# Kernel optimization log

Measured on AMD Instinct MI355X. Metric: run time of the kernel, lower is better.

## Reference

```python
import jax, jax.numpy as jnp
import numpy as np

B, T, W, L, H = 32, 1024, 512, 12, 8
CH = W // H                      # per-head dim = 64
IN_CH = 3 + 6 + T                # x + params + class embedding channels = 1033
DFF = 4 * W
NEG = -100000.0
SCALE = 1.0 / np.sqrt(np.sqrt(CH))


def _layernorm(x, g, b, eps=1e-5):
    m = jnp.mean(x, axis=-1, keepdims=True)
    v = jnp.mean(jnp.square(x - m), axis=-1, keepdims=True)
    return (x - m) * jax.lax.rsqrt(v + eps) * g + b


def setup_inputs() -> dict:
    key = jax.random.key(0)
    ks = jax.random.split(key, 40)
    std = 0.25 * np.sqrt(1.0 / W)  # init_scale used inside Transformer

    def n(k, shape, s=std):
        return (jax.random.normal(k, shape, jnp.float32) * s).astype(jnp.float32)

    inp = {
        'x': jax.random.normal(ks[0], (B, 3, T), jnp.float32),
        'params': jax.random.normal(ks[1], (B, 6, T), jnp.float32),
        'mask': (jax.random.uniform(ks[2], (B, T)) > 0.2).astype(jnp.float32),
        'class_emb': jax.random.normal(ks[3], (T, T), jnp.float32),  # nn.Embedding(n_ctx, n_ctx)
        'w_in': n(ks[4], (IN_CH, W), 0.02), 'b_in': jnp.zeros((W,), jnp.float32),
        'ln_pre_g': jnp.ones((W,), jnp.float32), 'ln_pre_b': jnp.zeros((W,), jnp.float32),
        'qkv_w': n(ks[5], (L, W, 3 * W)), 'qkv_b': jnp.zeros((L, 3 * W), jnp.float32),
        'attn_pw': n(ks[6], (L, W, W)), 'attn_pb': jnp.zeros((L, W), jnp.float32),
        'ln1_g': jnp.ones((L, W), jnp.float32), 'ln1_b': jnp.zeros((L, W), jnp.float32),
        'fc_w': n(ks[7], (L, W, DFF)), 'fc_b': jnp.zeros((L, DFF), jnp.float32),
        'fcp_w': n(ks[8], (L, DFF, W)), 'fcp_b': jnp.zeros((L, W), jnp.float32),
        'ln2_g': jnp.ones((L, W), jnp.float32), 'ln2_b': jnp.zeros((L, W), jnp.float32),
        'ln_post_g': jnp.ones((W,), jnp.float32), 'ln_post_b': jnp.zeros((W,), jnp.float32),
        'w_out': n(ks[9], (W, W), 0.02), 'b_out': jnp.zeros((W,), jnp.float32),
        'agg_fc_w': n(ks[10], (W, DFF)), 'agg_fc_b': jnp.zeros((DFF,), jnp.float32),
        'agg_pw': n(ks[11], (DFF, W)), 'agg_pb': jnp.zeros((W,), jnp.float32),
    }
    return inp


def _block(h, p):
    qw, qb, pw, pb, l1g, l1b, fw, fb, gw, gb, l2g, l2b = p
    hn = _layernorm(h, l1g, l1b)
    qkv = (hn @ qw + qb).reshape(B, T, H, 3 * CH)
    q, k, v = jnp.split(qkv, 3, axis=-1)
    att = jnp.einsum('bthc,bshc->bhts', q * SCALE, k * SCALE)
    att = jax.nn.softmax(att.astype(jnp.float32), axis=-1)  # softmax in fp32
    o = jnp.einsum('bhts,bshc->bthc', att, v).reshape(B, T, W)
    h = h + o @ pw + pb
    hn2 = _layernorm(h, l2g, l2b)
    h = h + jax.nn.gelu(hn2 @ fw + fb, approximate=False) @ gw + gb
    return h, None


def reference(x, params, mask, class_emb, w_in, b_in, ln_pre_g, ln_pre_b,
              qkv_w, qkv_b, attn_pw, attn_pb, ln1_g, ln1_b, fc_w, fc_b,
              fcp_w, fcp_b, ln2_g, ln2_b, ln_post_g, ln_post_b, w_out, b_out,
              agg_fc_w, agg_fc_b, agg_pw, agg_pb):
    # concatenate params and class-embedding channels: [B, 1033, T]
    ce = jnp.broadcast_to(class_emb.T[None], (B, T, T))  # class_embed.transpose(1,2)
    xin = jnp.concatenate([x, params, ce], axis=1)
    h = jnp.einsum('bct,cw->btw', xin, w_in) + b_in      # input_proj on [B,T,1033]
    h = _layernorm(h, ln_pre_g, ln_pre_b)
    h, _ = jax.lax.scan(_block, h,
                        (qkv_w, qkv_b, attn_pw, attn_pb, ln1_g, ln1_b,
                         fc_w, fc_b, fcp_w, fcp_b, ln2_g, ln2_b))
    h = _layernorm(h, ln_post_g, ln_post_b)
    h = (h @ w_out + b_out).transpose(0, 2, 1)           # [B, 512, T]
    h = h * mask[:, None, :]
    pooled = jnp.max(h + (1.0 - mask[:, None, :]) * NEG, axis=2)  # [B, 512]
    z = jax.nn.gelu(pooled @ agg_fc_w + agg_fc_b, approximate=False) @ agg_pw + agg_pb
    return (z, h)
```

## Files before the change

kernel.cpp:

```cpp
#include <hip/hip_runtime.h>
#include <hip/hip_bf16.h>


typedef unsigned short u16;
typedef unsigned int u32;
typedef __attribute__((ext_vector_type(8))) short bf16x8;
typedef __attribute__((ext_vector_type(8))) unsigned short us8;
typedef __attribute__((ext_vector_type(4))) unsigned short us4;
typedef __attribute__((ext_vector_type(4))) float f32x4;

__device__ __forceinline__ float bf2f(u16 s) {
  union { u32 u; float f; } c; c.u = ((u32)s) << 16; return c.f;
}
__device__ __forceinline__ u16 f2bf(float f) {
  __hip_bfloat16 h = __float2bfloat16(f);
  union { __hip_bfloat16 h; u16 u; } c; c.h = h; return c.u;
}
__device__ __forceinline__ float gelu_f(float v) {
  return 0.5f * v * (1.0f + erff(v * 0.7071067811865475f));
}
__device__ __forceinline__ void gl2lds16(const u16* g, u16* l) {
  __builtin_amdgcn_global_load_lds((const __attribute__((address_space(1))) void*)g,
                                   (__attribute__((address_space(3))) void*)l, 16, 0, 0);
}
__device__ __forceinline__ f32x4 mfma16(bf16x8 a, bf16x8 b, f32x4 c) {
  return __builtin_amdgcn_mfma_f32_16x16x32_bf16(a, b, c, 0, 0, 0);
}
__device__ __forceinline__ int swz(int row) { return (row ^ (row >> 3)) & 7; }

template <int EPI>
__global__ __launch_bounds__(512)
void gemm_bt(const u16* __restrict__ A, const u16* __restrict__ Bt,
             const float* __restrict__ bias, float* __restrict__ Cf,
             u16* __restrict__ Cb, u16* __restrict__ Vt, int K, int lda, int ldb, int ldc)
{
  __shared__ __align__(16) u16 As[2][256 * 32];
  __shared__ __align__(16) u16 Bs[2][128 * 32];
  const int tid = threadIdx.x;
  const int lane = tid & 63, wid = tid >> 6;
  const int wm = wid & 3, wn = wid >> 2;
  const int nbx = gridDim.x;
  const int nwg = nbx * gridDim.y;
  int lin = blockIdx.y * nbx + blockIdx.x;
  lin = (lin & 7) * (nwg >> 3) + (lin >> 3);
  const long m0 = (long)(lin / nbx) * 256, n0 = (long)(lin % nbx) * 128;

  const int c0 = tid, c1 = tid + 512;
  const int kc0 = (c0 & 3) ^ (((c0 >> 2) >> 1) & 3);
  const int kc1 = (c1 & 3) ^ (((c1 >> 2) >> 1) & 3);
  const int kcb = (tid & 3) ^ (((tid >> 2) >> 1) & 3);
  const u16* aS0 = A + (m0 + (c0 >> 2)) * (long)lda + kc0 * 8;
  const u16* aS1 = A + (m0 + (c1 >> 2)) * (long)lda + kc1 * 8;
  const u16* bS0 = Bt + (n0 + (tid >> 2)) * (long)ldb + kcb * 8;

  f32x4 acc[4][4] = {};
  const int cl4 = lane & 15;
  const int gph = ((lane >> 4) ^ ((cl4 >> 1) & 3)) * 8;
  const int aro = (wm * 64 + cl4) * 32 + gph;
  const int bro = (wn * 64 + cl4) * 32 + gph;
  const int nt = K >> 5;

#define STAGE_AB(buf, k0_)                          \
  gl2lds16(aS0 + (k0_), As[buf] + c0 * 8);          \
  gl2lds16(aS1 + (k0_), As[buf] + c1 * 8);          \
  gl2lds16(bS0 + (k0_), Bs[buf] + tid * 8);

  STAGE_AB(0, 0);
  for (int t = 0; t < nt; ++t) {
    const int cur = t & 1;
    if (t < nt - 1) {
      STAGE_AB(cur ^ 1, (t + 1) * 32);
      asm volatile("s_waitcnt vmcnt(3)" ::: "memory");
    } else {
      asm volatile("s_waitcnt vmcnt(0)" ::: "memory");
    }
    __builtin_amdgcn_s_barrier();
    bf16x8 af[4], bfr[4];
#pragma unroll
    for (int i = 0; i < 4; ++i) af[i] = *(const bf16x8*)(As[cur] + aro + i * 16 * 32);
#pragma unroll
    for (int j = 0; j < 4; ++j) bfr[j] = *(const bf16x8*)(Bs[cur] + bro + j * 16 * 32);
    __builtin_amdgcn_s_setprio(1);
#pragma unroll
    for (int i = 0; i < 4; ++i)
#pragma unroll
      for (int j = 0; j < 4; ++j)
        acc[i][j] = mfma16(af[i], bfr[j], acc[i][j]);
    __builtin_amdgcn_s_setprio(0);
    __builtin_amdgcn_s_barrier();
  }
#undef STAGE_AB
  const int rg = (lane >> 4) * 4, cl = lane & 15;
#pragma unroll
  for (int i = 0; i < 4; ++i) {
#pragma unroll
    for (int j = 0; j < 4; ++j) {
      const long row = m0 + wm * 64 + i * 16 + rg;
      const long col = n0 + wn * 64 + j * 16 + cl;
      const float bv = bias ? bias[col] : 0.0f;
      if (EPI == 4) {
        const int hh = (int)col / 192, off = (int)col - hh * 192;
        if (off < 64) {
#pragma unroll
          for (int r = 0; r < 4; ++r)
            Cb[(row + r) * ldc + col] = f2bf((acc[i][j][r] + bv) * 0.125f);
        } else if (off < 128) {
#pragma unroll
          for (int r = 0; r < 4; ++r)
            Cb[(row + r) * ldc + col] = f2bf(acc[i][j][r] + bv);
        } else {
          us4 pk;
#pragma unroll
          for (int r = 0; r < 4; ++r) pk[r] = f2bf(acc[i][j][r] + bv);
          const long bl = row >> 10, t0 = row & 1023;
          *(us4*)(Vt + (((bl * 8 + hh) * 64 + (off - 128)) << 10) + t0) = pk;
        }
      } else {
#pragma unroll
        for (int r = 0; r < 4; ++r) {
          float v = acc[i][j][r] + bv;
          long idx = (row + r) * ldc + col;
          if (EPI == 0) Cf[idx] = v;
          else if (EPI == 1) Cb[idx] = f2bf(v);
          else if (EPI == 2) Cf[idx] += v;
          else Cb[idx] = f2bf(gelu_f(v));
        }
      }
    }
  }
}

template <int EPI>
__global__ __launch_bounds__(256)
void gemm_bt1(const u16* __restrict__ A, const u16* __restrict__ Bt,
              const float* __restrict__ bias, float* __restrict__ Cf,
              u16* __restrict__ Cb, int K, int lda, int ldb, int ldc)
{
  __shared__ __align__(16) u16 As[2][128 * 32];
  __shared__ __align__(16) u16 Bs[2][128 * 32];
  const int tid = threadIdx.x;
  const int lane = tid & 63, wid = tid >> 6;
  const int wm = wid >> 1, wn = wid & 1;
  const int nbx = gridDim.x;
  const int nwg = nbx * gridDim.y;
  int lin = blockIdx.y * nbx + blockIdx.x;
  lin = (lin & 7) * (nwg >> 3) + (lin >> 3);
  const long m0 = (long)(lin / nbx) * 128, n0 = (long)(lin % nbx) * 128;

  const int c0 = tid, c1 = tid + 256;
  const int kc0 = (c0 & 3) ^ (((c0 >> 2) >> 1) & 3);
  const int kc1 = (c1 & 3) ^ (((c1 >> 2) >> 1) & 3);
  const u16* aS0 = A + (m0 + (c0 >> 2)) * (long)lda + kc0 * 8;
  const u16* aS1 = A + (m0 + (c1 >> 2)) * (long)lda + kc1 * 8;
  const u16* bS0 = Bt + (n0 + (c0 >> 2)) * (long)ldb + kc0 * 8;
  const u16* bS1 = Bt + (n0 + (c1 >> 2)) * (long)ldb + kc1 * 8;

  f32x4 acc[4][4] = {};
  const int cl4 = lane & 15;
  const int gph = ((lane >> 4) ^ ((cl4 >> 1) & 3)) * 8;
  const int aro = (wm * 64 + cl4) * 32 + gph;
  const int bro = (wn * 64 + cl4) * 32 + gph;
  const int nt = K >> 5;

#define STAGE_AB1(buf, k0_)                         \
  gl2lds16(aS0 + (k0_), As[buf] + c0 * 8);          \
  gl2lds16(aS1 + (k0_), As[buf] + c1 * 8);          \
  gl2lds16(bS0 + (k0_), Bs[buf] + c0 * 8);          \
  gl2lds16(bS1 + (k0_), Bs[buf] + c1 * 8);

  STAGE_AB1(0, 0);
  for (int t = 0; t < nt; ++t) {
    const int cur = t & 1;
    if (t < nt - 1) {
      STAGE_AB1(cur ^ 1, (t + 1) * 32);
      asm volatile("s_waitcnt vmcnt(4)" ::: "memory");
    } else {
      asm volatile("s_waitcnt vmcnt(0)" ::: "memory");
    }
    __builtin_amdgcn_s_barrier();
    bf16x8 af[4], bfr[4];
#pragma unroll
    for (int i = 0; i < 4; ++i) af[i] = *(const bf16x8*)(As[cur] + aro + i * 16 * 32);
#pragma unroll
    for (int j = 0; j < 4; ++j) bfr[j] = *(const bf16x8*)(Bs[cur] + bro + j * 16 * 32);
    __builtin_amdgcn_s_setprio(1);
#pragma unroll
    for (int i = 0; i < 4; ++i)
#pragma unroll
      for (int j = 0; j < 4; ++j)
        acc[i][j] = mfma16(af[i], bfr[j], acc[i][j]);
    __builtin_amdgcn_s_setprio(0);
    __builtin_amdgcn_s_barrier();
  }
#undef STAGE_AB1
  const int rg = (lane >> 4) * 4, cl = lane & 15;
#pragma unroll
  for (int i = 0; i < 4; ++i) {
#pragma unroll
    for (int j = 0; j < 4; ++j) {
      const long row = m0 + wm * 64 + i * 16 + rg;
      const long col = n0 + wn * 64 + j * 16 + cl;
      const float bv = bias ? bias[col] : 0.0f;
#pragma unroll
      for (int r = 0; r < 4; ++r) {
        float v = acc[i][j][r] + bv;
        long idx = (row + r) * ldc + col;
        if (EPI == 0) Cf[idx] = v;
        else if (EPI == 1) Cb[idx] = f2bf(v);
        else if (EPI == 2) Cf[idx] += v;
        else Cb[idx] = f2bf(gelu_f(v));
      }
    }
  }
}

template <int EPI>
__global__ __launch_bounds__(1024)
void gemm_bt2(const u16* __restrict__ A, const u16* __restrict__ Bt,
              const float* __restrict__ bias, float* __restrict__ Cf,
              u16* __restrict__ Cb, int K, int lda, int ldb, int ldc)
{
  __shared__ __align__(16) u16 As[2][256 * 32];
  __shared__ __align__(16) u16 Bs[2][256 * 32];
  const int tid = threadIdx.x;
  const int lane = tid & 63, wid = tid >> 6;
  const int wm = wid & 3, wn = wid >> 2;
  const int nbx = gridDim.x;
  const int nwg = nbx * gridDim.y;
  int lin = blockIdx.y * nbx + blockIdx.x;
  lin = (lin & 7) * (nwg >> 3) + (lin >> 3);
  const long m0 = (long)(lin / nbx) * 256, n0 = (long)(lin % nbx) * 256;

  const int kcA = (tid & 3) ^ (((tid >> 2) >> 1) & 3);
  const u16* aS0 = A + (m0 + (tid >> 2)) * (long)lda + kcA * 8;
  const u16* bS0 = Bt + (n0 + (tid >> 2)) * (long)ldb + kcA * 8;

  f32x4 acc[4][4] = {};
  const int cl4 = lane & 15;
  const int gph = ((lane >> 4) ^ ((cl4 >> 1) & 3)) * 8;
  const int aro = (wm * 64 + cl4) * 32 + gph;
  const int bro = (wn * 64 + cl4) * 32 + gph;
  const int nt = K >> 5;

#define STAGE_AB2(buf, k0_)                         \
  gl2lds16(aS0 + (k0_), As[buf] + tid * 8);         \
  gl2lds16(bS0 + (k0_), Bs[buf] + tid * 8);

  STAGE_AB2(0, 0);
  for (int t = 0; t < nt; ++t) {
    const int cur = t & 1;
    if (t < nt - 1) {
      STAGE_AB2(cur ^ 1, (t + 1) * 32);
      asm volatile("s_waitcnt vmcnt(2)" ::: "memory");
    } else {
      asm volatile("s_waitcnt vmcnt(0)" ::: "memory");
    }
    __builtin_amdgcn_s_barrier();
    bf16x8 af[4], bfr[4];
#pragma unroll
    for (int i = 0; i < 4; ++i) af[i] = *(const bf16x8*)(As[cur] + aro + i * 16 * 32);
#pragma unroll
    for (int j = 0; j < 4; ++j) bfr[j] = *(const bf16x8*)(Bs[cur] + bro + j * 16 * 32);
    __builtin_amdgcn_s_setprio(1);
#pragma unroll
    for (int i = 0; i < 4; ++i)
#pragma unroll
      for (int j = 0; j < 4; ++j)
        acc[i][j] = mfma16(af[i], bfr[j], acc[i][j]);
    __builtin_amdgcn_s_setprio(0);
    __builtin_amdgcn_s_barrier();
  }
#undef STAGE_AB2
  const int rg = (lane >> 4) * 4, cl = lane & 15;
#pragma unroll
  for (int i = 0; i < 4; ++i) {
#pragma unroll
    for (int j = 0; j < 4; ++j) {
      const long row = m0 + wm * 64 + i * 16 + rg;
      const long col = n0 + wn * 64 + j * 16 + cl;
      const float bv = bias ? bias[col] : 0.0f;
#pragma unroll
      for (int r = 0; r < 4; ++r) {
        float v = acc[i][j][r] + bv;
        long idx = (row + r) * ldc + col;
        if (EPI == 0) Cf[idx] = v;
        else if (EPI == 1) Cb[idx] = f2bf(v);
        else if (EPI == 2) Cf[idx] += v;
        else Cb[idx] = f2bf(gelu_f(v));
      }
    }
  }
}

__global__ __launch_bounds__(512)
void attn_k(const u16* __restrict__ qkv, const u16* __restrict__ vt, u16* __restrict__ o)
{
  __shared__ __align__(16) u16 Ks[2][64 * 64];
  __shared__ __align__(16) u16 Vts[2][64 * 64];
  __shared__ __align__(16) u16 Ps[8][512];
  const int tid = threadIdx.x, lane = tid & 63, wid = tid >> 6;
  int lin = blockIdx.x;
  lin = (lin & 7) * 128 + (lin >> 3);
  const int qt = lin & 7, hh = (lin >> 3) & 7, b = lin >> 6;
  const long rowbase = (long)b * 1024;
  const long vbase = (((long)b * 8 + hh) * 64) * 1024;
  const int g = lane >> 4, cl = lane & 15;
  u16* Psw = Ps[wid];
  const int Rq = wid * 16 + cl;
  const int sw2 = ((cl >> 1) & 3) << 3;

  bf16x8 aq[2];
  {
    const u16* qp = qkv + (rowbase + qt * 128 + Rq) * 1536 + hh * 192 + g * 8;
    aq[0] = *(const bf16x8*)(qp);
    aq[1] = *(const bf16x8*)(qp + 32);
  }
#define STAGE_KV(buf, kt_)                                                            \
  {                                                                                   \
    int row = tid >> 3, c8s = (tid & 7) ^ swz(row);                                   \
    gl2lds16(qkv + (rowbase + (kt_) * 64 + row) * 1536 + hh * 192 + 64 + c8s * 8,     \
             Ks[buf] + tid * 8);                                                      \
    gl2lds16(vt + vbase + (long)row * 1024 + (kt_) * 64 + c8s * 8, Vts[buf] + tid * 8); \
  }
  STAGE_KV(0, 0);

  float m = -3.0e38f, l = 0.f;
  f32x4 oacc[4] = {};

  for (int kt = 0; kt < 16; ++kt) {
    const int cur = kt & 1;
    if (kt < 15) {
      STAGE_KV(cur ^ 1, kt + 1);
      asm volatile("s_waitcnt vmcnt(2)" ::: "memory");
    } else {
      asm volatile("s_waitcnt vmcnt(0)" ::: "memory");
    }
    __builtin_amdgcn_s_barrier();
    f32x4 s[4] = {};
    __builtin_amdgcn_s_setprio(1);
#pragma unroll
    for (int j = 0; j < 4; ++j) {
      const int Rk = j * 16 + cl, sk = swz(Rk) << 3;
#pragma unroll
      for (int kb = 0; kb < 2; ++kb) {
        bf16x8 bk = *(const bf16x8*)(Ks[cur] + Rk * 64 + ((kb * 32 + g * 8) ^ sk));
        s[j] = mfma16(bk, aq[kb], s[j]);
      }
    }
    __builtin_amdgcn_s_setprio(0);
    float mx = s[0][0];
#pragma unroll
    for (int j = 0; j < 4; ++j)
#pragma unroll
      for (int r = 0; r < 4; ++r) mx = fmaxf(mx, s[j][r]);
    mx = fmaxf(mx, __shfl_xor(mx, 16, 64));
    mx = fmaxf(mx, __shfl_xor(mx, 32, 64));
    if (!__all(mx <= m + 8.f)) {
      const float mnew = fmaxf(m, mx);
      const float al = __expf(m - mnew);
      m = mnew;
      l *= al;
      float alr[4];
#pragma unroll
      for (int r = 0; r < 4; ++r) alr[r] = __shfl(al, (lane & 48) | (g * 4 + r), 64);
#pragma unroll
      for (int cb = 0; cb < 4; ++cb) {
        f32x4 t = oacc[cb];
        t[0] *= alr[0]; t[1] *= alr[1]; t[2] *= alr[2]; t[3] *= alr[3];
        oacc[cb] = t;
      }
    }
    float p[4][4], ts = 0.f;
#pragma unroll
    for (int j = 0; j < 4; ++j)
#pragma unroll
      for (int r = 0; r < 4; ++r) {
        p[j][r] = __expf(s[j][r] - m);
        ts += p[j][r];
      }
    ts += __shfl_xor(ts, 16, 64);
    ts += __shfl_xor(ts, 32, 64);
    l += ts;
#pragma unroll
    for (int kb = 0; kb < 2; ++kb) {
#pragma unroll
      for (int jj = 0; jj < 2; ++jj) {
        us4 pk;
        pk[0] = f2bf(p[2 * kb + jj][0]); pk[1] = f2bf(p[2 * kb + jj][1]);
        pk[2] = f2bf(p[2 * kb + jj][2]); pk[3] = f2bf(p[2 * kb + jj][3]);
        *(us4*)(&Psw[cl * 32 + ((jj * 16 + g * 4) ^ sw2)]) = pk;
      }
      asm volatile("s_waitcnt lgkmcnt(0)" ::: "memory");
      bf16x8 pa = *(const bf16x8*)(&Psw[cl * 32 + ((g * 8) ^ sw2)]);
      __builtin_amdgcn_s_setprio(1);
#pragma unroll
      for (int cb = 0; cb < 4; ++cb) {
        const int ch = cb * 16 + cl;
        bf16x8 vb = *(const bf16x8*)(Vts[cur] + ch * 64 + ((kb * 32 + g * 8) ^ (swz(ch) << 3)));
        oacc[cb] = mfma16(pa, vb, oacc[cb]);
      }
      __builtin_amdgcn_s_setprio(0);
    }
    __builtin_amdgcn_s_barrier();
  }
#undef STAGE_KV
  float lr[4];
#pragma unroll
  for (int r = 0; r < 4; ++r) lr[r] = __shfl(l, (lane & 48) | (g * 4 + r), 64);
#pragma unroll
  for (int cb = 0; cb < 4; ++cb)
#pragma unroll
    for (int r = 0; r < 4; ++r) {
      long row = rowbase + qt * 128 + wid * 16 + g * 4 + r;
      o[row * 512 + hh * 64 + cb * 16 + cl] = f2bf(oacc[cb][r] / lr[r]);
    }
}

template <int MODE>
__global__ __launch_bounds__(256)
void ln_k(const float* __restrict__ in_, const float* __restrict__ gg,
          const float* __restrict__ bb, void* __restrict__ out_)
{
  const long row = (long)blockIdx.x * 4 + (threadIdx.x >> 6);
  const int lane = threadIdx.x & 63;
  float x[8];
  const float* p = in_ + row * 512 + lane * 8;
  *(float4*)(x) = *(const float4*)(p);
  *(float4*)(x + 4) = *(const float4*)(p + 4);
  float s = 0.f;
#pragma unroll
  for (int j = 0; j < 8; ++j) s += x[j];
#pragma unroll
  for (int off = 1; off < 64; off <<= 1) s += __shfl_xor(s, off, 64);
  const float mean = s * (1.0f / 512.0f);
  float vs = 0.f;
#pragma unroll
  for (int j = 0; j < 8; ++j) { float d = x[j] - mean; vs += d * d; }
#pragma unroll
  for (int off = 1; off < 64; off <<= 1) vs += __shfl_xor(vs, off, 64);
  const float rstd = rsqrtf(vs * (1.0f / 512.0f) + 1e-5f);
  if (MODE == 0) {
    float y[8];
#pragma unroll
    for (int j = 0; j < 8; ++j)
      y[j] = (x[j] - mean) * rstd * gg[lane * 8 + j] + bb[lane * 8 + j];
    float* q = (float*)out_ + row * 512 + lane * 8;
    *(float4*)(q) = *(const float4*)(y);
    *(float4*)(q + 4) = *(const float4*)(y + 4);
  } else {
    us8 ov;
#pragma unroll
    for (int j = 0; j < 8; ++j)
      ov[j] = f2bf((x[j] - mean) * rstd * gg[lane * 8 + j] + bb[lane * 8 + j]);
    *(us8*)((u16*)out_ + row * 512 + lane * 8) = ov;
  }
}

__global__ __launch_bounds__(256)
void embed_ln_k(const float* __restrict__ x, const float* __restrict__ par,
                const float* __restrict__ E, const float* __restrict__ w_in,
                const float* __restrict__ b_in, const float* __restrict__ gg,
                const float* __restrict__ bb, float* __restrict__ h)
{
  __shared__ float red[8];
  const long bt = blockIdx.x;
  const int b = (int)(bt >> 10), t = (int)(bt & 1023);
  const int tid = threadIdx.x, lane = tid & 63, wid = tid >> 6;
  float xs[9];
#pragma unroll
  for (int c = 0; c < 3; ++c) xs[c] = x[((long)b * 3 + c) * 1024 + t];
#pragma unroll
  for (int c = 0; c < 6; ++c) xs[3 + c] = par[((long)b * 6 + c) * 1024 + t];
  float a[2];
#pragma unroll
  for (int ii = 0; ii < 2; ++ii) {
    const int w = tid + ii * 256;
    float v = E[(long)t * 512 + w] + b_in[w];
#pragma unroll
    for (int c = 0; c < 9; ++c) v += xs[c] * w_in[c * 512 + w];
    a[ii] = v;
  }
  float s = a[0] + a[1];
#pragma unroll
  for (int off = 1; off < 64; off <<= 1) s += __shfl_xor(s, off, 64);
  if (lane == 0) red[wid] = s;
  __syncthreads();
  const float mean = (red[0] + red[1] + red[2] + red[3]) * (1.0f / 512.0f);
  float d0 = a[0] - mean, d1 = a[1] - mean;
  float vs = d0 * d0 + d1 * d1;
#pragma unroll
  for (int off = 1; off < 64; off <<= 1) vs += __shfl_xor(vs, off, 64);
  if (lane == 0) red[4 + wid] = vs;
  __syncthreads();
  const float rstd = rsqrtf((red[4] + red[5] + red[6] + red[7]) * (1.0f / 512.0f) + 1e-5f);
#pragma unroll
  for (int ii = 0; ii < 2; ++ii) {
    const int w = tid + ii * 256;
    h[bt * 512 + w] = (a[ii] - mean) * rstd * gg[w] + bb[w];
  }
}

__global__ __launch_bounds__(256)
void tr_k(const float* __restrict__ in, u16* __restrict__ out, int R, int C)
{
  __shared__ u16 tile[32][33];
  const int r0 = blockIdx.y * 32, c0 = blockIdx.x * 32;
  const int tx = threadIdx.x & 31, ty = threadIdx.x >> 5;
  for (int rr = ty; rr < 32; rr += 8) tile[rr][tx] = f2bf(in[(long)(r0 + rr) * C + c0 + tx]);
  __syncthreads();
  for (int rr = ty; rr < 32; rr += 8) out[(long)(c0 + rr) * R + r0 + tx] = tile[tx][rr];
}

__global__ __launch_bounds__(256)
void trL_k(const float* __restrict__ qkv_w, const float* __restrict__ pw,
           const float* __restrict__ fcw, const float* __restrict__ fcpw,
           u16* __restrict__ o_qkv, u16* __restrict__ o_pw,
           u16* __restrict__ o_fc, u16* __restrict__ o_fcp)
{
  __shared__ u16 tile[32][33];
  int bid = blockIdx.x;
  const float* src; u16* dst; int R, C, bx, by;
  if (bid < 768)       { src = qkv_w; dst = o_qkv; R = 512;  C = 1536; bx = bid % 48; by = bid / 48; }
  else if (bid < 1024) { bid -= 768;  src = pw;   dst = o_pw;  R = 512;  C = 512;  bx = bid % 16; by = bid / 16; }
  else if (bid < 2048) { bid -= 1024; src = fcw;  dst = o_fc;  R = 512;  C = 2048; bx = bid % 64; by = bid / 64; }
  else                 { bid -= 2048; src = fcpw; dst = o_fcp; R = 2048; C = 512;  bx = bid % 16; by = bid / 16; }
  const int r0 = by * 32, c0 = bx * 32;
  const int tx = threadIdx.x & 31, ty = threadIdx.x >> 5;
  for (int rr = ty; rr < 32; rr += 8) tile[rr][tx] = f2bf(src[(long)(r0 + rr) * C + c0 + tx]);
  __syncthreads();
  for (int rr = ty; rr < 32; rr += 8) dst[(long)(c0 + rr) * R + r0 + tx] = tile[tx][rr];
}

__global__ __launch_bounds__(256)
void cast_k(const float* __restrict__ in, u16* __restrict__ out, long n)
{
  long i = ((long)blockIdx.x * 256 + threadIdx.x) * 4;
  if (i + 3 < n) {
    float4 v = *(const float4*)(in + i);
    out[i] = f2bf(v.x); out[i + 1] = f2bf(v.y); out[i + 2] = f2bf(v.z); out[i + 3] = f2bf(v.w);
  }
}

__global__ __launch_bounds__(256)
void tout_k(const float* __restrict__ hm, const float* __restrict__ mask,
            float* __restrict__ outh, float* __restrict__ part)
{
  __shared__ float tile[64][65];
  const int bx = blockIdx.x;
  const int t0 = bx * 64, w0 = blockIdx.y * 64, b = blockIdx.z;
  const int tx = threadIdx.x & 63, ty = threadIdx.x >> 6;
  for (int i = ty; i < 64; i += 4)
    tile[i][tx] = hm[((long)b * 1024 + t0 + i) * 512 + w0 + tx];
  __syncthreads();
  const float mv = mask[b * 1024 + t0 + tx];
  const float neg = (1.0f - mv) * (-100000.0f);
  for (int i = ty; i < 64; i += 4) {
    const float v = tile[tx][i] * mv;
    outh[((long)b * 512 + w0 + i) * 1024 + t0 + tx] = v;
    float pm = v + neg;
#pragma unroll
    for (int off = 1; off < 64; off <<= 1) pm = fmaxf(pm, __shfl_xor(pm, off, 64));
    if (tx == 0) part[(((long)b * 16 + bx) * 512) + w0 + i] = pm;
  }
}
__global__ __launch_bounds__(256)
void pool2_k(const float* __restrict__ part, float* __restrict__ pooled)
{
  const int b = blockIdx.y;
  const int w = blockIdx.x * 256 + threadIdx.x;
  float m = -3.0e38f;
#pragma unroll
  for (int c = 0; c < 16; ++c) m = fmaxf(m, part[((long)b * 16 + c) * 512 + w]);
  pooled[b * 512 + w] = m;
}

__global__ __launch_bounds__(256)
void agg1p_k(const float* __restrict__ pooled, const float* __restrict__ wf,
             float* __restrict__ part)
{
  const int b = blockIdx.z, kc = blockIdx.y;
  const int n = blockIdx.x * 256 + threadIdx.x;
  float acc = 0.f;
  const int k0 = kc * 64;
#pragma unroll 8
  for (int k = 0; k < 64; ++k) acc += pooled[b * 512 + k0 + k] * wf[(long)(k0 + k) * 2048 + n];
  part[((long)b * 8 + kc) * 2048 + n] = acc;
}
__global__ __launch_bounds__(256)
void agg1c_k(const float* __restrict__ part, const float* __restrict__ bf_,
             float* __restrict__ z1)
{
  const int b = blockIdx.y;
  const int n = blockIdx.x * 256 + threadIdx.x;
  float acc = 0.f;
#pragma unroll
  for (int c = 0; c < 8; ++c) acc += part[((long)b * 8 + c) * 2048 + n];
  z1[(long)b * 2048 + n] = gelu_f(acc + bf_[n]);
}
__global__ __launch_bounds__(256)
void agg2p_k(const float* __restrict__ z1, const float* __restrict__ wp,
             float* __restrict__ part)
{
  const int b = blockIdx.z, kc = blockIdx.y;
  const int n = blockIdx.x * 256 + threadIdx.x;
  float acc = 0.f;
  const int k0 = kc * 256;
#pragma unroll 8
  for (int k = 0; k < 256; ++k) acc += z1[(long)b * 2048 + k0 + k] * wp[(long)(k0 + k) * 512 + n];
  part[((long)b * 8 + kc) * 512 + n] = acc;
}
__global__ __launch_bounds__(256)
void agg2c_k(const float* __restrict__ part, const float* __restrict__ bp,
             float* __restrict__ zo)
{
  const int b = blockIdx.y;
  const int n = blockIdx.x * 256 + threadIdx.x;
  float acc = 0.f;
#pragma unroll
  for (int c = 0; c < 8; ++c) acc += part[((long)b * 8 + c) * 512 + n];
  zo[b * 512 + n] = acc + bp[n];
}

extern "C" void kernel_launch(void* const* d_in, const int* in_sizes, int n_in,
                              void* d_out, int out_size, void* d_ws, size_t ws_size,
                              hipStream_t stream)
{
  (void)in_sizes; (void)n_in; (void)out_size; (void)ws_size;
  const float* x        = (const float*)d_in[0];
  const float* params   = (const float*)d_in[1];
  const float* mask     = (const float*)d_in[2];
  const float* class_emb= (const float*)d_in[3];
  const float* w_in     = (const float*)d_in[4];
  const float* b_in     = (const float*)d_in[5];
  const float* ln_pre_g = (const float*)d_in[6];
  const float* ln_pre_b = (const float*)d_in[7];
  const float* qkv_w    = (const float*)d_in[8];
  const float* qkv_b    = (const float*)d_in[9];
  const float* attn_pw  = (const float*)d_in[10];
  const float* attn_pb  = (const float*)d_in[11];
  const float* ln1_g    = (const float*)d_in[12];
  const float* ln1_b    = (const float*)d_in[13];
  const float* fc_w     = (const float*)d_in[14];
  const float* fc_b     = (const float*)d_in[15];
  const float* fcp_w    = (const float*)d_in[16];
  const float* fcp_b    = (const float*)d_in[17];
  const float* ln2_g    = (const float*)d_in[18];
  const float* ln2_b    = (const float*)d_in[19];
  const float* ln_post_g= (const float*)d_in[20];
  const float* ln_post_b= (const float*)d_in[21];
  const float* w_out    = (const float*)d_in[22];
  const float* b_out    = (const float*)d_in[23];
  const float* agg_fc_w = (const float*)d_in[24];
  const float* agg_fc_b = (const float*)d_in[25];
  const float* agg_pw   = (const float*)d_in[26];
  const float* agg_pb   = (const float*)d_in[27];

  float* out_f = (float*)d_out;
  float* out_h = out_f + 16384;
  u16* sc = (u16*)out_h;

  char* ws = (char*)d_ws;
  float* hf = (float*)ws;       ws += (size_t)32768 * 512 * 4;
  u16* hn = (u16*)ws;           ws += (size_t)32768 * 512 * 2;
  float* E = (float*)ws;        ws += (size_t)1024 * 512 * 4;
  u16* ce_b = (u16*)ws;         ws += (size_t)1024 * 1024 * 2;
  u16* wt_qkv = (u16*)ws;       ws += (size_t)1536 * 512 * 2;
  u16* wt_pw  = (u16*)ws;       ws += (size_t)512 * 512 * 2;
  u16* wt_fc  = (u16*)ws;       ws += (size_t)2048 * 512 * 2;
  u16* wt_fcp = (u16*)ws;       ws += (size_t)512 * 2048 * 2;
  u16* w_in_t = (u16*)ws;       ws += (size_t)512 * 1024 * 2;
  u16* w_out_t= (u16*)ws;       ws += (size_t)512 * 512 * 2;
  float* pooled = (float*)ws;   ws += (size_t)32 * 512 * 4;
  float* z1     = (float*)ws;   ws += (size_t)32 * 2048 * 4;
  float* part   = (float*)ws;   ws += (size_t)32 * 16 * 512 * 4;
  float* apart1 = (float*)ws;   ws += (size_t)32 * 8 * 2048 * 4;
  float* apart2 = (float*)ws;   ws += (size_t)32 * 8 * 512 * 4;
  u16* vt       = (u16*)ws;     ws += (size_t)16 * 8 * 64 * 1024 * 2;

  cast_k<<<1024, 256, 0, stream>>>(class_emb, ce_b, 1024 * 1024);
  tr_k<<<dim3(16, 32), 256, 0, stream>>>(w_in + 9 * 512, w_in_t, 1024, 512);
  tr_k<<<dim3(16, 16), 256, 0, stream>>>(w_out, w_out_t, 512, 512);
  gemm_bt<0><<<dim3(4, 4), 512, 0, stream>>>(ce_b, w_in_t, nullptr, E, nullptr, nullptr,
                                             1024, 1024, 1024, 512);
  embed_ln_k<<<32768, 256, 0, stream>>>(x, params, E, w_in, b_in, ln_pre_g, ln_pre_b, hf);

  for (int l = 0; l < 12; ++l) {
    trL_k<<<3072, 256, 0, stream>>>(qkv_w + (size_t)l * 512 * 1536,
                                    attn_pw + (size_t)l * 512 * 512,
                                    fc_w + (size_t)l * 512 * 2048,
                                    fcp_w + (size_t)l * 2048 * 512,
                                    wt_qkv, wt_pw, wt_fc, wt_fcp);

    ln_k<1><<<8192, 256, 0, stream>>>(hf, ln1_g + l * 512, ln1_b + l * 512, hn);
    for (int half = 0; half < 2; ++half) {
      const size_t ro = (size_t)half * 16384;
      gemm_bt<4><<<dim3(12, 64), 512, 0, stream>>>(hn + ro * 512, wt_qkv, qkv_b + l * 1536,
                                                   nullptr, sc, vt, 512, 512, 512, 1536);
      attn_k<<<1024, 512, 0, stream>>>(sc, vt, hn + ro * 512);
    }
    gemm_bt1<2><<<dim3(4, 256), 256, 0, stream>>>(hn, wt_pw, attn_pb + l * 512,
                                                  hf, nullptr, 512, 512, 512, 512);
    ln_k<1><<<8192, 256, 0, stream>>>(hf, ln2_g + l * 512, ln2_b + l * 512, hn);
    for (int half = 0; half < 2; ++half) {
      const size_t ro = (size_t)half * 16384;
      gemm_bt2<3><<<dim3(8, 64), 1024, 0, stream>>>(hn + ro * 512, wt_fc, fc_b + l * 2048,
                                                    nullptr, sc, 512, 512, 512, 2048);
      gemm_bt1<2><<<dim3(4, 128), 256, 0, stream>>>(sc, wt_fcp, fcp_b + l * 512,
                                                    hf + ro * 512, nullptr, 2048, 2048, 2048, 512);
    }
  }

  ln_k<1><<<8192, 256, 0, stream>>>(hf, ln_post_g, ln_post_b, hn);
  gemm_bt1<0><<<dim3(4, 256), 256, 0, stream>>>(hn, w_out_t, b_out, hf, nullptr,
                                                512, 512, 512, 512);
  tout_k<<<dim3(16, 8, 32), 256, 0, stream>>>(hf, mask, out_h, part);
  pool2_k<<<dim3(2, 32), 256, 0, stream>>>(part, pooled);
  agg1p_k<<<dim3(8, 8, 32), 256, 0, stream>>>(pooled, agg_fc_w, apart1);
  agg1c_k<<<dim3(8, 32), 256, 0, stream>>>(apart1, agg_fc_b, z1);
  agg2p_k<<<dim3(2, 8, 32), 256, 0, stream>>>(z1, agg_pw, apart2);
  agg2c_k<<<dim3(2, 32), 256, 0, stream>>>(apart2, agg_pb, out_f);
}
```

Measured before the change: 6.678 ms.

## Swap attn-proj and output GEMMs to gemm_bt, split pooling from transpose

The attention projection and final output projection now use the larger-tile gemm_bt kernel (512 threads, half as many row blocks) in place of gemm_bt1. Pooling is split out of the transpose kernel into a separate pool1_k that reads row-major h directly and drops the wavefront shuffle reductions. The transposed output write is moved to the end, after the aggregation MLP. This aims at better GEMM efficiency and less shuffle work in the epilogue, at the cost of reading h one more time.

Result: faster. 6.422 ms (-3.8%).

```diff
diff --git a/kernel.cpp b/kernel.cpp
--- a/kernel.cpp
+++ b/kernel.cpp
@@ -542,36 +542,45 @@
 }
 
 __global__ __launch_bounds__(256)
-void tout_k(const float* __restrict__ hm, const float* __restrict__ mask,
-            float* __restrict__ outh, float* __restrict__ part)
+void pool1_k(const float* __restrict__ hm, const float* __restrict__ mask, float* __restrict__ part)
+{
+  const int c = blockIdx.x, b = blockIdx.y;
+  const int t0 = c * 128;
+  const int w0 = threadIdx.x, w1 = threadIdx.x + 256;
+  float m0 = -3.0e38f, m1 = -3.0e38f;
+  for (int t = 0; t < 128; ++t) {
+    const float mv = mask[b * 1024 + t0 + t];
+    const float neg = (1.0f - mv) * (-100000.0f);
+    const float* row = hm + ((long)b * 1024 + t0 + t) * 512;
+    m0 = fmaxf(m0, row[w0] * mv + neg);
+    m1 = fmaxf(m1, row[w1] * mv + neg);
+  }
+  part[((long)b * 8 + c) * 512 + w0] = m0;
+  part[((long)b * 8 + c) * 512 + w1] = m1;
+}
+__global__ __launch_bounds__(256)
+void pool2_k(const float* __restrict__ part, float* __restrict__ pooled)
+{
+  const int b = blockIdx.y;
+  const int w = blockIdx.x * 256 + threadIdx.x;
+  float m = -3.0e38f;
+#pragma unroll
+  for (int c = 0; c < 8; ++c) m = fmaxf(m, part[((long)b * 8 + c) * 512 + w]);
+  pooled[b * 512 + w] = m;
+}
+
+__global__ __launch_bounds__(256)
+void tout_k(const float* __restrict__ hm, const float* __restrict__ mask, float* __restrict__ outh)
 {
   __shared__ float tile[64][65];
-  const int bx = blockIdx.x;
-  const int t0 = bx * 64, w0 = blockIdx.y * 64, b = blockIdx.z;
+  const int t0 = blockIdx.x * 64, w0 = blockIdx.y * 64, b = blockIdx.z;
   const int tx = threadIdx.x & 63, ty = threadIdx.x >> 6;
   for (int i = ty; i < 64; i += 4)
     tile[i][tx] = hm[((long)b * 1024 + t0 + i) * 512 + w0 + tx];
   __syncthreads();
   const float mv = mask[b * 1024 + t0 + tx];
-  const float neg = (1.0f - mv) * (-100000.0f);
-  for (int i = ty; i < 64; i += 4) {
-    const float v = tile[tx][i] * mv;
-    outh[((long)b * 512 + w0 + i) * 1024 + t0 + tx] = v;
-    float pm = v + neg;
-#pragma unroll
-    for (int off = 1; off < 64; off <<= 1) pm = fmaxf(pm, __shfl_xor(pm, off, 64));
-    if (tx == 0) part[(((long)b * 16 + bx) * 512) + w0 + i] = pm;
-  }
-}
-__global__ __launch_bounds__(256)
-void pool2_k(const float* __restrict__ part, float* __restrict__ pooled)
-{
-  const int b = blockIdx.y;
-  const int w = blockIdx.x * 256 + threadIdx.x;
-  float m = -3.0e38f;
-#pragma unroll
-  for (int c = 0; c < 16; ++c) m = fmaxf(m, part[((long)b * 16 + c) * 512 + w]);
-  pooled[b * 512 + w] = m;
+  for (int i = ty; i < 64; i += 4)
+    outh[((long)b * 512 + w0 + i) * 1024 + t0 + tx] = tile[tx][i] * mv;
 }
 
 __global__ __launch_bounds__(256)
@@ -672,7 +681,7 @@
   u16* w_out_t= (u16*)ws;       ws += (size_t)512 * 512 * 2;
   float* pooled = (float*)ws;   ws += (size_t)32 * 512 * 4;
   float* z1     = (float*)ws;   ws += (size_t)32 * 2048 * 4;
-  float* part   = (float*)ws;   ws += (size_t)32 * 16 * 512 * 4;
+  float* part   = (float*)ws;   ws += (size_t)32 * 8 * 512 * 4;
   float* apart1 = (float*)ws;   ws += (size_t)32 * 8 * 2048 * 4;
   float* apart2 = (float*)ws;   ws += (size_t)32 * 8 * 512 * 4;
   u16* vt       = (u16*)ws;     ws += (size_t)16 * 8 * 64 * 1024 * 2;
@@ -698,8 +707,8 @@
                                                    nullptr, sc, vt, 512, 512, 512, 1536);
       attn_k<<<1024, 512, 0, stream>>>(sc, vt, hn + ro * 512);
     }
-    gemm_bt1<2><<<dim3(4, 256), 256, 0, stream>>>(hn, wt_pw, attn_pb + l * 512,
-                                                  hf, nullptr, 512, 512, 512, 512);
+    gemm_bt<2><<<dim3(4, 128), 512, 0, stream>>>(hn, wt_pw, attn_pb + l * 512,
+                                                 hf, nullptr, nullptr, 512, 512, 512, 512);
     ln_k<1><<<8192, 256, 0, stream>>>(hf, ln2_g + l * 512, ln2_b + l * 512, hn);
     for (int half = 0; half < 2; ++half) {
       const size_t ro = (size_t)half * 16384;
@@ -711,12 +720,13 @@
   }
 
   ln_k<1><<<8192, 256, 0, stream>>>(hf, ln_post_g, ln_post_b, hn);
-  gemm_bt1<0><<<dim3(4, 256), 256, 0, stream>>>(hn, w_out_t, b_out, hf, nullptr,
-                                                512, 512, 512, 512);
-  tout_k<<<dim3(16, 8, 32), 256, 0, stream>>>(hf, mask, out_h, part);
+  gemm_bt<0><<<dim3(4, 128), 512, 0, stream>>>(hn, w_out_t, b_out, hf, nullptr, nullptr,
+                                               512, 512, 512, 512);
+  pool1_k<<<dim3(8, 32), 256, 0, stream>>>(hf, mask, part);
   pool2_k<<<dim3(2, 32), 256, 0, stream>>>(part, pooled);
   agg1p_k<<<dim3(8, 8, 32), 256, 0, stream>>>(pooled, agg_fc_w, apart1);
   agg1c_k<<<dim3(8, 32), 256, 0, stream>>>(apart1, agg_fc_b, z1);
   agg2p_k<<<dim3(2, 8, 32), 256, 0, stream>>>(z1, agg_pw, apart2);
   agg2c_k<<<dim3(2, 32), 256, 0, stream>>>(apart2, agg_pb, out_f);
-}
+  tout_k<<<dim3(16, 8, 32), 256, 0, stream>>>(hf, mask, out_h);
+}
```
